# Kernel optimization log

Hardware: AMD Instinct MI355X
Metric: run time of the kernel (lower is better)

The kernel has to match this reference:

```python
import jax, jax.numpy as jnp
import numpy as np

Z, P, CIN, COUT, E, HID = 4, 512, 32, 32, 65536, 128

def setup_inputs() -> dict:
    key = jax.random.key(0)
    ks = jax.random.split(key, 8)
    return {
        "features": jax.random.normal(ks[0], (Z, P, CIN), dtype=jnp.float32),
        "edge_vec": jax.random.normal(ks[1], (E, 3), dtype=jnp.float32),
        "W1": jax.random.normal(ks[2], (4, HID), dtype=jnp.float32) * 0.5,
        "b1": jax.random.normal(ks[3], (HID,), dtype=jnp.float32) * 0.1,
        "W2": jax.random.normal(ks[4], (HID, COUT * CIN), dtype=jnp.float32) * (1.0 / np.sqrt(HID)),
        "edge_batch": jax.random.randint(ks[5], (E,), 0, Z),
        "edge_a": jax.random.randint(ks[6], (E,), 0, P),
        "edge_b": jax.random.randint(ks[7], (E,), 0, P),
        "n_norm": 1,
    }

def reference(features, edge_vec, W1, b1, W2, edge_batch, edge_a, edge_b, n_norm):
    Zb, Pn, Cin = features.shape
    # zero near-degenerate radii (matches radius[norm < 1e-10] = 0)
    r = jnp.linalg.norm(edge_vec, axis=-1, keepdims=True)  # [E,1]
    vec = jnp.where(r < 1e-10, jnp.zeros_like(edge_vec), edge_vec)
    rn = jnp.where(r < 1e-10, jnp.zeros_like(r), r)
    # per-edge kernel: MLP(vec, |vec|) -> [E, c_out, c_in]
    x = jnp.concatenate([vec, rn], axis=-1)               # [E,4]
    h = jax.nn.relu(x @ W1 + b1)                          # [E,HID]
    Cout = W2.shape[1] // Cin
    k = (h @ W2).reshape(-1, Cout, Cin)                   # [E,co,ci]
    # gather neighbor features, per-edge matvec, scatter-add to centers
    f_b = features[edge_batch, edge_b]                    # [E,ci]
    msg = jnp.einsum('eij,ej->ei', k, f_b)                # [E,co]
    seg = edge_batch * Pn + edge_a
    out = jax.ops.segment_sum(msg, seg, num_segments=Zb * Pn)
    out = out.reshape(Zb, Pn, Cout)
    return out / jnp.sqrt(jnp.asarray(n_norm, dtype=features.dtype))
```

## Files before the change

kernel.cpp:

```cpp
#include <hip/hip_runtime.h>
#include <hip/hip_bf16.h>

#define ZBATCH 4
#define PN     512
#define CINC   32
#define COUTC  32
#define EN     65536
#define HIDN   128
#define NNODE  (ZBATCH*PN)
#define JD     (HIDN*COUTC)
#define CAP    128

__global__ __launch_bounds__(256) void k1_bin_wf(
    const float* __restrict__ F, const float* __restrict__ W2,
    __hip_bfloat16* __restrict__ Wf, const int* __restrict__ eb,
    const int* __restrict__ ea, const int* __restrict__ ebn,
    int* __restrict__ cnt_src, int* __restrict__ cnt_dst,
    int* __restrict__ order_src, int* __restrict__ order_dst) {
  const int t = threadIdx.x;
  const int b = blockIdx.x;
  if (b < 256) {
    const int e = b * 256 + t;
    const int zb = eb[e];
    const int ns = zb * PN + ebn[e];
    const int nd = zb * PN + ea[e];
    const int p = atomicAdd(&cnt_src[ns], 1);
    if (p < CAP) order_src[ns * CAP + p] = e;
    const int q = atomicAdd(&cnt_dst[nd], 1);
    if (q < CAP) order_dst[nd * CAP + q] = e;
    return;
  }
  const int bb = b - 256;
  const int j = (bb & 15) * 256 + t;
  const int n0 = (bb >> 4) * 16;
  const int h = j >> 5, co = j & 31;
  const float4* w4 = (const float4*)(W2 + h * (COUTC * CINC) + co * CINC);
  float w[32];
#pragma unroll
  for (int q = 0; q < 8; ++q) {
    const float4 x = w4[q];
    w[4 * q] = x.x; w[4 * q + 1] = x.y; w[4 * q + 2] = x.z; w[4 * q + 3] = x.w;
  }
  for (int n = 0; n < 16; ++n) {
    const float* fr = F + (size_t)(n0 + n) * CINC;
    float acc = 0.f;
#pragma unroll
    for (int ci = 0; ci < 32; ++ci) acc = fmaf(fr[ci], w[ci], acc);
    Wf[(size_t)(n0 + n) * JD + j] = __float2bfloat16(acc);
  }
}

__global__ __launch_bounds__(256) void k2_msg(
    const float* __restrict__ evec, const float* __restrict__ W1,
    const float* __restrict__ b1, const __hip_bfloat16* __restrict__ Wf,
    const int* __restrict__ cnt_src, const int* __restrict__ order_src,
    const int* __restrict__ nn, float* __restrict__ msg) {
  const int n = blockIdx.x;
  const int t = threadIdx.x;
  const int lane = t & 63, w = t >> 6;
  const int co = lane & 31, hh = lane >> 5;

  __shared__ float w1s[4][HIDN];
  __shared__ float b1s[HIDN];
  __shared__ int ords[CAP];
  __shared__ __align__(16) float Hbuf[4][8][HIDN];

  const int c0 = cnt_src[n];
  const int count = c0 < CAP ? c0 : CAP;
  if (count == 0) return;

  for (int i = t; i < 4 * HIDN; i += 256) w1s[i >> 7][i & 127] = W1[i];
  for (int i = t; i < HIDN; i += 256) b1s[i] = b1[i];
  if (t < count) ords[t] = order_src[(size_t)n * CAP + t];

  float wf[64];
  {
    const __hip_bfloat16* wp = Wf + (size_t)n * JD + hh * 64 * COUTC + co;
#pragma unroll
    for (int j = 0; j < 64; ++j) wf[j] = __bfloat162float(wp[(size_t)j * COUTC]);
  }
  const float scale = rsqrtf((float)nn[0]);
  __syncthreads();

  const int h0 = lane << 1;
  for (int base = w * 8; base < count; base += 32) {
    int e8[8]; float ex[8], ey[8], ez[8];
#pragma unroll
    for (int i = 0; i < 8; ++i) {
      const int idx = (base + i < count) ? (base + i) : (count - 1);
      e8[i] = ords[idx];
    }
#pragma unroll
    for (int i = 0; i < 8; ++i) {
      ex[i] = evec[3 * e8[i]];
      ey[i] = evec[3 * e8[i] + 1];
      ez[i] = evec[3 * e8[i] + 2];
    }
#pragma unroll
    for (int i = 0; i < 8; ++i) {
      const float r = sqrtf(ex[i] * ex[i] + ey[i] * ey[i] + ez[i] * ez[i]);
      const bool bad = (r < 1e-10f);
      const float y0 = bad ? 0.f : ex[i], y1 = bad ? 0.f : ey[i];
      const float y2 = bad ? 0.f : ez[i], y3 = bad ? 0.f : r;
      float a0 = b1s[h0]     + y0 * w1s[0][h0]     + y1 * w1s[1][h0]
                             + y2 * w1s[2][h0]     + y3 * w1s[3][h0];
      float a1 = b1s[h0 + 1] + y0 * w1s[0][h0 + 1] + y1 * w1s[1][h0 + 1]
                             + y2 * w1s[2][h0 + 1] + y3 * w1s[3][h0 + 1];
      float2 hv;
      hv.x = fmaxf(a0, 0.f);
      hv.y = fmaxf(a1, 0.f);
      *(float2*)(&Hbuf[w][i][h0]) = hv;
    }
    __builtin_amdgcn_wave_barrier();
#pragma unroll
    for (int i = 0; i < 8; ++i) {
      const float4* hp = (const float4*)(&Hbuf[w][i][hh * 64]);
      float a0 = 0.f, a1 = 0.f, a2 = 0.f, a3 = 0.f;
#pragma unroll
      for (int k = 0; k < 4; ++k) {
        const float4 p0 = hp[4 * k + 0];
        const float4 p1 = hp[4 * k + 1];
        const float4 p2 = hp[4 * k + 2];
        const float4 p3 = hp[4 * k + 3];
        a0 = fmaf(p0.x, wf[16 * k + 0], a0);  a0 = fmaf(p0.y, wf[16 * k + 1], a0);
        a0 = fmaf(p0.z, wf[16 * k + 2], a0);  a0 = fmaf(p0.w, wf[16 * k + 3], a0);
        a1 = fmaf(p1.x, wf[16 * k + 4], a1);  a1 = fmaf(p1.y, wf[16 * k + 5], a1);
        a1 = fmaf(p1.z, wf[16 * k + 6], a1);  a1 = fmaf(p1.w, wf[16 * k + 7], a1);
        a2 = fmaf(p2.x, wf[16 * k + 8], a2);  a2 = fmaf(p2.y, wf[16 * k + 9], a2);
        a2 = fmaf(p2.z, wf[16 * k + 10], a2); a2 = fmaf(p2.w, wf[16 * k + 11], a2);
        a3 = fmaf(p3.x, wf[16 * k + 12], a3); a3 = fmaf(p3.y, wf[16 * k + 13], a3);
        a3 = fmaf(p3.z, wf[16 * k + 14], a3); a3 = fmaf(p3.w, wf[16 * k + 15], a3);
      }
      float acc = (a0 + a1) + (a2 + a3);
      acc += __shfl_xor(acc, 32);
      if (hh == 0 && base + i < count)
        msg[(size_t)e8[i] * COUTC + co] = acc * scale;
    }
    __builtin_amdgcn_wave_barrier();
  }
}

__global__ __launch_bounds__(256) void k3_reduce(
    const float* __restrict__ msg, const int* __restrict__ cnt_dst,
    const int* __restrict__ order_dst, float* __restrict__ out) {
  const int t = threadIdx.x;
  const int lane = t & 63, w = t >> 6;
  const int co = lane & 31, hh = lane >> 5;
  const int n = blockIdx.x * 4 + w;
  __shared__ int idxs[4][CAP];
  const int c0 = cnt_dst[n];
  const int count = c0 < CAP ? c0 : CAP;
  for (int i = lane; i < count; i += 64)
    idxs[w][i] = order_dst[(size_t)n * CAP + i];
  __builtin_amdgcn_wave_barrier();
  float a0 = 0.f, a1 = 0.f, a2 = 0.f, a3 = 0.f;
  for (int g = hh * 4; g < count; g += 8) {
    const int i1 = g + 1, i2 = g + 2, i3 = g + 3;
    a0 += msg[(size_t)idxs[w][g] * COUTC + co];
    if (i1 < count) a1 += msg[(size_t)idxs[w][i1] * COUTC + co];
    if (i2 < count) a2 += msg[(size_t)idxs[w][i2] * COUTC + co];
    if (i3 < count) a3 += msg[(size_t)idxs[w][i3] * COUTC + co];
  }
  float acc = (a0 + a1) + (a2 + a3);
  acc += __shfl_xor(acc, 32);
  if (hh == 0) out[(size_t)n * COUTC + co] = acc;
}

extern "C" void kernel_launch(void* const* d_in, const int* in_sizes, int n_in,
                              void* d_out, int out_size, void* d_ws, size_t ws_size,
                              hipStream_t stream) {
  const float* features   = (const float*)d_in[0];
  const float* edge_vec   = (const float*)d_in[1];
  const float* W1         = (const float*)d_in[2];
  const float* b1         = (const float*)d_in[3];
  const float* W2         = (const float*)d_in[4];
  const int*   edge_batch = (const int*)d_in[5];
  const int*   edge_a     = (const int*)d_in[6];
  const int*   edge_b     = (const int*)d_in[7];
  const int*   n_norm     = (const int*)d_in[8];
  float* out = (float*)d_out;

  char* ws = (char*)d_ws;
  __hip_bfloat16* Wf = (__hip_bfloat16*)ws;
  float* msg = (float*)(ws + (size_t)NNODE * JD * 2);
  int* ints = (int*)(ws + (size_t)NNODE * JD * 2 + (size_t)EN * COUTC * 4);
  int* cnt_src   = ints;
  int* cnt_dst   = ints + NNODE;
  int* order_src = ints + 2 * NNODE;
  int* order_dst = order_src + NNODE * CAP;
  const size_t need = (size_t)NNODE * JD * 2 + (size_t)EN * COUTC * 4
                    + (size_t)(2 * NNODE + 2 * NNODE * CAP) * 4;
  if (ws_size < need) return;

  hipMemsetAsync(cnt_src, 0, 2 * NNODE * 4, stream);
  k1_bin_wf<<<256 + 2048, 256, 0, stream>>>(features, W2, Wf, edge_batch,
                                            edge_a, edge_b, cnt_src, cnt_dst,
                                            order_src, order_dst);
  k2_msg<<<NNODE, 256, 0, stream>>>(edge_vec, W1, b1, Wf, cnt_src, order_src,
                                    n_norm, msg);
  k3_reduce<<<NNODE / 4, 256, 0, stream>>>(msg, cnt_dst, order_dst, out);
}
```

Before: 144.6 us.

## Switch per-node fused weights to packed fp16 with fdot2 and vectorized layout

The precomputed per-node fused weight matrix changes from bf16 stored in [h][co] order to packed fp16 pairs laid out as [co][hidden-pair]. Each k2 thread can then load its weights with wide uint4 loads instead of 64 strided scalar loads. The hidden activations are packed to fp16 in shared memory, and the 128-wide contraction uses v_dot2 fp16 instructions, halving both the FMA count and the LDS traffic. W1 and b1 now live in registers instead of shared memory, and k1 is restructured to produce two hidden rows per thread over 32-node tiles. The cost is fp16 rounding of activations and weights, and reduced range compared with bf16.

```diff
diff --git a/kernel.cpp b/kernel.cpp
--- a/kernel.cpp
+++ b/kernel.cpp
@@ -1,5 +1,4 @@
 #include <hip/hip_runtime.h>
-#include <hip/hip_bf16.h>
 
 #define ZBATCH 4
 #define PN     512
@@ -8,12 +7,35 @@
 #define EN     65536
 #define HIDN   128
 #define NNODE  (ZBATCH*PN)
-#define JD     (HIDN*COUTC)
 #define CAP    128
+#define HP     64
+#define WFW    (HP*COUTC)
+
+using hvec2 = decltype(__builtin_amdgcn_cvt_pkrtz(0.f, 0.f));
+
+static __device__ __forceinline__ unsigned packh2(float a, float b) {
+  hvec2 h = __builtin_amdgcn_cvt_pkrtz(a, b);
+  unsigned u;
+  __builtin_memcpy(&u, &h, 4);
+  return u;
+}
+
+static __device__ __forceinline__ float dot2acc(unsigned hu, unsigned wu,
+                                                float acc) {
+  hvec2 a, b;
+  __builtin_memcpy(&a, &hu, 4);
+  __builtin_memcpy(&b, &wu, 4);
+#if __has_builtin(__builtin_amdgcn_fdot2)
+  return __builtin_amdgcn_fdot2(a, b, acc, false);
+#else
+  acc = fmaf((float)a.x, (float)b.x, acc);
+  return fmaf((float)a.y, (float)b.y, acc);
+#endif
+}
 
 __global__ __launch_bounds__(256) void k1_bin_wf(
     const float* __restrict__ F, const float* __restrict__ W2,
-    __hip_bfloat16* __restrict__ Wf, const int* __restrict__ eb,
+    unsigned* __restrict__ Wf, const int* __restrict__ eb,
     const int* __restrict__ ea, const int* __restrict__ ebn,
     int* __restrict__ cnt_src, int* __restrict__ cnt_dst,
     int* __restrict__ order_src, int* __restrict__ order_dst) {
@@ -31,28 +53,37 @@
     return;
   }
   const int bb = b - 256;
-  const int j = (bb & 15) * 256 + t;
-  const int n0 = (bb >> 4) * 16;
-  const int h = j >> 5, co = j & 31;
-  const float4* w4 = (const float4*)(W2 + h * (COUTC * CINC) + co * CINC);
-  float w[32];
-#pragma unroll
-  for (int q = 0; q < 8; ++q) {
-    const float4 x = w4[q];
-    w[4 * q] = x.x; w[4 * q + 1] = x.y; w[4 * q + 2] = x.z; w[4 * q + 3] = x.w;
-  }
-  for (int n = 0; n < 16; ++n) {
-    const float* fr = F + (size_t)(n0 + n) * CINC;
-    float acc = 0.f;
-#pragma unroll
-    for (int ci = 0; ci < 32; ++ci) acc = fmaf(fr[ci], w[ci], acc);
-    Wf[(size_t)(n0 + n) * JD + j] = __float2bfloat16(acc);
+  const int jt = bb & 7, ntile = bb >> 3;
+  const int hp = t & 63;
+  const int co = jt * 4 + (t >> 6);
+  const float4* rA = (const float4*)(W2 + (size_t)(2 * hp) * (COUTC * CINC)
+                                     + co * CINC);
+  const float4* rB = (const float4*)(W2 + (size_t)(2 * hp + 1) * (COUTC * CINC)
+                                     + co * CINC);
+  float4 wa[8], wb[8];
+#pragma unroll
+  for (int q = 0; q < 8; ++q) { wa[q] = rA[q]; wb[q] = rB[q]; }
+  const int n0 = ntile * 32;
+  for (int n = 0; n < 32; ++n) {
+    const float4* fr = (const float4*)(F + (size_t)(n0 + n) * CINC);
+    float a0 = 0.f, a1 = 0.f, a2 = 0.f, a3 = 0.f;
+    float c0 = 0.f, c1 = 0.f, c2 = 0.f, c3 = 0.f;
+#pragma unroll
+    for (int q = 0; q < 8; ++q) {
+      const float4 f = fr[q];
+      a0 = fmaf(f.x, wa[q].x, a0); a1 = fmaf(f.y, wa[q].y, a1);
+      a2 = fmaf(f.z, wa[q].z, a2); a3 = fmaf(f.w, wa[q].w, a3);
+      c0 = fmaf(f.x, wb[q].x, c0); c1 = fmaf(f.y, wb[q].y, c1);
+      c2 = fmaf(f.z, wb[q].z, c2); c3 = fmaf(f.w, wb[q].w, c3);
+    }
+    Wf[(size_t)(n0 + n) * WFW + co * HP + hp] =
+        packh2((a0 + a1) + (a2 + a3), (c0 + c1) + (c2 + c3));
   }
 }
 
 __global__ __launch_bounds__(256) void k2_msg(
     const float* __restrict__ evec, const float* __restrict__ W1,
-    const float* __restrict__ b1, const __hip_bfloat16* __restrict__ Wf,
+    const float* __restrict__ b1, const unsigned* __restrict__ Wf,
     const int* __restrict__ cnt_src, const int* __restrict__ order_src,
     const int* __restrict__ nn, float* __restrict__ msg) {
   const int n = blockIdx.x;
@@ -60,29 +91,29 @@
   const int lane = t & 63, w = t >> 6;
   const int co = lane & 31, hh = lane >> 5;
 
-  __shared__ float w1s[4][HIDN];
-  __shared__ float b1s[HIDN];
   __shared__ int ords[CAP];
-  __shared__ __align__(16) float Hbuf[4][8][HIDN];
+  __shared__ __align__(16) unsigned Hbuf[4][8][64];
 
   const int c0 = cnt_src[n];
   const int count = c0 < CAP ? c0 : CAP;
   if (count == 0) return;
 
-  for (int i = t; i < 4 * HIDN; i += 256) w1s[i >> 7][i & 127] = W1[i];
-  for (int i = t; i < HIDN; i += 256) b1s[i] = b1[i];
+  uint4 wfv[8];
+  {
+    const uint4* wp = (const uint4*)(Wf + (size_t)n * WFW + co * HP + hh * 32);
+#pragma unroll
+    for (int q = 0; q < 8; ++q) wfv[q] = wp[q];
+  }
   if (t < count) ords[t] = order_src[(size_t)n * CAP + t];
-
-  float wf[64];
-  {
-    const __hip_bfloat16* wp = Wf + (size_t)n * JD + hh * 64 * COUTC + co;
-#pragma unroll
-    for (int j = 0; j < 64; ++j) wf[j] = __bfloat162float(wp[(size_t)j * COUTC]);
-  }
+  const int h0 = lane << 1;
+  const float2 u0 = *(const float2*)(W1 + 0 * HIDN + h0);
+  const float2 u1 = *(const float2*)(W1 + 1 * HIDN + h0);
+  const float2 u2 = *(const float2*)(W1 + 2 * HIDN + h0);
+  const float2 u3 = *(const float2*)(W1 + 3 * HIDN + h0);
+  const float2 b2 = *(const float2*)(b1 + h0);
   const float scale = rsqrtf((float)nn[0]);
   __syncthreads();
 
-  const int h0 = lane << 1;
   for (int base = w * 8; base < count; base += 32) {
     int e8[8]; float ex[8], ey[8], ez[8];
 #pragma unroll
@@ -102,36 +133,26 @@
       const bool bad = (r < 1e-10f);
       const float y0 = bad ? 0.f : ex[i], y1 = bad ? 0.f : ey[i];
       const float y2 = bad ? 0.f : ez[i], y3 = bad ? 0.f : r;
-      float a0 = b1s[h0]     + y0 * w1s[0][h0]     + y1 * w1s[1][h0]
-                             + y2 * w1s[2][h0]     + y3 * w1s[3][h0];
-      float a1 = b1s[h0 + 1] + y0 * w1s[0][h0 + 1] + y1 * w1s[1][h0 + 1]
-                             + y2 * w1s[2][h0 + 1] + y3 * w1s[3][h0 + 1];
-      float2 hv;
-      hv.x = fmaxf(a0, 0.f);
-      hv.y = fmaxf(a1, 0.f);
-      *(float2*)(&Hbuf[w][i][h0]) = hv;
+      const float a0 = fmaf(y3, u3.x, fmaf(y2, u2.x,
+                       fmaf(y1, u1.x, fmaf(y0, u0.x, b2.x))));
+      const float a1 = fmaf(y3, u3.y, fmaf(y2, u2.y,
+                       fmaf(y1, u1.y, fmaf(y0, u0.y, b2.y))));
+      Hbuf[w][i][lane] = packh2(fmaxf(a0, 0.f), fmaxf(a1, 0.f));
     }
     __builtin_amdgcn_wave_barrier();
 #pragma unroll
     for (int i = 0; i < 8; ++i) {
-      const float4* hp = (const float4*)(&Hbuf[w][i][hh * 64]);
-      float a0 = 0.f, a1 = 0.f, a2 = 0.f, a3 = 0.f;
-#pragma unroll
-      for (int k = 0; k < 4; ++k) {
-        const float4 p0 = hp[4 * k + 0];
-        const float4 p1 = hp[4 * k + 1];
-        const float4 p2 = hp[4 * k + 2];
-        const float4 p3 = hp[4 * k + 3];
-        a0 = fmaf(p0.x, wf[16 * k + 0], a0);  a0 = fmaf(p0.y, wf[16 * k + 1], a0);
-        a0 = fmaf(p0.z, wf[16 * k + 2], a0);  a0 = fmaf(p0.w, wf[16 * k + 3], a0);
-        a1 = fmaf(p1.x, wf[16 * k + 4], a1);  a1 = fmaf(p1.y, wf[16 * k + 5], a1);
-        a1 = fmaf(p1.z, wf[16 * k + 6], a1);  a1 = fmaf(p1.w, wf[16 * k + 7], a1);
-        a2 = fmaf(p2.x, wf[16 * k + 8], a2);  a2 = fmaf(p2.y, wf[16 * k + 9], a2);
-        a2 = fmaf(p2.z, wf[16 * k + 10], a2); a2 = fmaf(p2.w, wf[16 * k + 11], a2);
-        a3 = fmaf(p3.x, wf[16 * k + 12], a3); a3 = fmaf(p3.y, wf[16 * k + 13], a3);
-        a3 = fmaf(p3.z, wf[16 * k + 14], a3); a3 = fmaf(p3.w, wf[16 * k + 15], a3);
+      const uint4* hp4 = (const uint4*)&Hbuf[w][i][hh * 32];
+      float s0 = 0.f, s1 = 0.f, s2 = 0.f, s3 = 0.f;
+#pragma unroll
+      for (int q = 0; q < 8; ++q) {
+        const uint4 hv = hp4[q];
+        s0 = dot2acc(hv.x, wfv[q].x, s0);
+        s1 = dot2acc(hv.y, wfv[q].y, s1);
+        s2 = dot2acc(hv.z, wfv[q].z, s2);
+        s3 = dot2acc(hv.w, wfv[q].w, s3);
       }
-      float acc = (a0 + a1) + (a2 + a3);
+      float acc = (s0 + s1) + (s2 + s3);
       acc += __shfl_xor(acc, 32);
       if (hh == 0 && base + i < count)
         msg[(size_t)e8[i] * COUTC + co] = acc * scale;
@@ -181,21 +202,21 @@
   float* out = (float*)d_out;
 
   char* ws = (char*)d_ws;
-  __hip_bfloat16* Wf = (__hip_bfloat16*)ws;
-  float* msg = (float*)(ws + (size_t)NNODE * JD * 2);
-  int* ints = (int*)(ws + (size_t)NNODE * JD * 2 + (size_t)EN * COUTC * 4);
+  unsigned* Wf = (unsigned*)ws;
+  float* msg = (float*)(ws + (size_t)NNODE * WFW * 4);
+  int* ints = (int*)(ws + (size_t)NNODE * WFW * 4 + (size_t)EN * COUTC * 4);
   int* cnt_src   = ints;
   int* cnt_dst   = ints + NNODE;
   int* order_src = ints + 2 * NNODE;
   int* order_dst = order_src + NNODE * CAP;
-  const size_t need = (size_t)NNODE * JD * 2 + (size_t)EN * COUTC * 4
+  const size_t need = (size_t)NNODE * WFW * 4 + (size_t)EN * COUTC * 4
                     + (size_t)(2 * NNODE + 2 * NNODE * CAP) * 4;
   if (ws_size < need) return;
 
-  hipMemsetAsync(cnt_src, 0, 2 * NNODE * 4, stream);
-  k1_bin_wf<<<256 + 2048, 256, 0, stream>>>(features, W2, Wf, edge_batch,
-                                            edge_a, edge_b, cnt_src, cnt_dst,
-                                            order_src, order_dst);
+  (void)hipMemsetAsync(cnt_src, 0, 2 * NNODE * 4, stream);
+  k1_bin_wf<<<256 + 512, 256, 0, stream>>>(features, W2, Wf, edge_batch,
+                                           edge_a, edge_b, cnt_src, cnt_dst,
+                                           order_src, order_dst);
   k2_msg<<<NNODE, 256, 0, stream>>>(edge_vec, W1, b1, Wf, cnt_src, order_src,
                                     n_norm, msg);
   k3_reduce<<<NNODE / 4, 256, 0, stream>>>(msg, cnt_dst, order_dst, out);
```

After: 141.1 us. -2.4%, faster.
